# Kernel tuning notes

Hardware: AMD Instinct MI355X
Metric: run time of the kernel (lower is better)

The kernel has to match this reference:

```python
import jax, jax.numpy as jnp
import numpy as np

HIDDEN = 256
HEADS = 8
HEAD_DIM = HIDDEN // HEADS
SCALE = HEAD_DIM ** -0.5
N = 4096
NUM_GRAPHS = 16
LN_EPS = 1e-5


def setup_inputs() -> dict:
    key = jax.random.key(0)
    ks = jax.random.split(key, 8)
    x = jax.random.normal(ks[0], (N, HIDDEN), dtype=jnp.float32)
    batch = jnp.sort(jax.random.randint(ks[1], (N,), 0, NUM_GRAPHS, dtype=jnp.int64))
    # Xavier-uniform linear weights, stored as [in, out] (y = x @ W + b)
    lim = float(np.sqrt(6.0 / (HIDDEN + HIDDEN)))
    def W(k):
        return jax.random.uniform(k, (HIDDEN, HIDDEN), jnp.float32, -lim, lim)
    return {
        "x": x,
        "batch": batch,
        "Wq": W(ks[2]), "bq": jnp.zeros((HIDDEN,), jnp.float32),
        "Wk": W(ks[3]), "bk": jnp.zeros((HIDDEN,), jnp.float32),
        "Wv": W(ks[4]), "bv": jnp.zeros((HIDDEN,), jnp.float32),
        "Wo": W(ks[5]), "bo": jnp.zeros((HIDDEN,), jnp.float32),
        "gamma": jnp.ones((HIDDEN,), jnp.float32),
        "beta": jnp.zeros((HIDDEN,), jnp.float32),
    }


def _layer_norm(x, gamma, beta):
    mu = jnp.mean(x, axis=-1, keepdims=True)
    var = jnp.mean(jnp.square(x - mu), axis=-1, keepdims=True)
    return (x - mu) * jax.lax.rsqrt(var + LN_EPS) * gamma + beta


def reference(x, batch, Wq, bq, Wk, bk, Wv, bv, Wo, bo, gamma, beta):
    residual = x
    h = _layer_norm(x, gamma, beta)
    n = h.shape[0]
    q = (h @ Wq + bq).reshape(n, HEADS, HEAD_DIM)
    k = (h @ Wk + bk).reshape(n, HEADS, HEAD_DIM)
    v = (h @ Wv + bv).reshape(n, HEADS, HEAD_DIM)
    # dense scores masked to block-diagonal (same-graph) structure
    scores = jnp.einsum('ihd,jhd->ihj', q, k) * SCALE  # [N, H, N]
    same_graph = (batch[None, :] == batch[:, None])[:, None, :]  # [N, 1, N]
    scores = jnp.where(same_graph, scores, -jnp.inf)
    attn = jax.nn.softmax(scores, axis=-1)
    attn = jnp.nan_to_num(attn, nan=0.0)
    out = jnp.einsum('ihj,jhd->ihd', attn, v).reshape(n, HIDDEN)
    out = out @ Wo + bo
    return residual + out
```

## Files before the change

### kernel.cpp

```cpp
#include <hip/hip_runtime.h>

#define NNODES 4096
#define HID 256
#define NG 16
#define NH 8
#define HD 32
#define LN_EPS 1e-5f
#define QSCALE (0.17677669529663687f * 1.4426950408889634f)
#define CAPT 384
#define KLS 40
#define VTS (CAPT + 2)

typedef unsigned short u16;
typedef unsigned int u32;
typedef __bf16 bf16x8 __attribute__((ext_vector_type(8)));
typedef float f32x4 __attribute__((ext_vector_type(4)));

__device__ __forceinline__ float bf2f(u16 u){
  union { u32 i; float f; } c; c.i = ((u32)u) << 16; return c.f;
}
__device__ __forceinline__ u16 f2bf(float f){
  union { float f; u32 i; } c; c.f = f;
  u32 x = c.i;
  return (u16)((x + 0x7fffu + ((x >> 16) & 1u)) >> 16);
}

__global__ __launch_bounds__(256) void prep_kernel(
    const float* __restrict__ x, const float* __restrict__ gamma,
    const float* __restrict__ beta, u16* __restrict__ h,
    const float* __restrict__ Wq, const float* __restrict__ Wk,
    const float* __restrict__ Wv, const float* __restrict__ Wo,
    u16* __restrict__ Wt, const int* __restrict__ bw, int* __restrict__ seg){
  __shared__ u16 tile[32][33];
  __shared__ int bad;
  int b = blockIdx.x;
  if (b < 1024){
    int wave = threadIdx.x >> 6, lane = threadIdx.x & 63;
    int row = b * 4 + wave;
    float4 xv = ((const float4*)x)[row * 64 + lane];
    float a0 = xv.x, a1 = xv.y, a2 = xv.z, a3 = xv.w;
    float s = a0 + a1 + a2 + a3;
    #pragma unroll
    for (int m = 1; m < 64; m <<= 1) s += __shfl_xor(s, m);
    float mu = s * (1.0f / HID);
    float d0 = a0 - mu, d1 = a1 - mu, d2 = a2 - mu, d3 = a3 - mu;
    float vv = d0*d0 + d1*d1 + d2*d2 + d3*d3;
    #pragma unroll
    for (int m = 1; m < 64; m <<= 1) vv += __shfl_xor(vv, m);
    float rs = rsqrtf(vv * (1.0f / HID) + LN_EPS);
    float4 gv = ((const float4*)gamma)[lane];
    float4 bv = ((const float4*)beta)[lane];
    ushort4 o;
    o.x = f2bf(d0 * rs * gv.x + bv.x);
    o.y = f2bf(d1 * rs * gv.y + bv.y);
    o.z = f2bf(d2 * rs * gv.z + bv.z);
    o.w = f2bf(d3 * rs * gv.w + bv.w);
    *(ushort4*)(h + (size_t)row * HID + lane * 4) = o;
  } else if (b < 1280){
    int idx = b - 1024;
    int w = idx >> 6;
    int t = idx & 63;
    int bx = (t & 7) * 32, by = (t >> 3) * 32;
    const float* src = (w == 0) ? Wq : (w == 1) ? Wk : (w == 2) ? Wv : Wo;
    u16* dst = Wt + (size_t)w * HID * HID;
    int tx = threadIdx.x & 31, ty = threadIdx.x >> 5;
    #pragma unroll
    for (int r = 0; r < 32; r += 8)
      tile[ty + r][tx] = f2bf(src[(size_t)(by + ty + r) * HID + bx + tx]);
    __syncthreads();
    #pragma unroll
    for (int r = 0; r < 32; r += 8)
      dst[(size_t)(bx + ty + r) * HID + by + tx] = tile[tx][ty + r];
  } else {
    if (threadIdx.x == 0) bad = 0;
    __syncthreads();
    int local_bad = 0;
    for (int i = threadIdx.x; i < NNODES; i += 256){
      int v = bw[i];
      if (v < 0 || v > 15) local_bad = 1;
      if (i + 1 < NNODES && bw[i + 1] < v) local_bad = 1;
    }
    if (local_bad) atomicOr(&bad, 1);
    __syncthreads();
    int stride = bad ? 2 : 1;
    int g = threadIdx.x;
    if (g <= NG){
      int lo = 0, hi = NNODES;
      while (lo < hi){
        int mid = (lo + hi) >> 1;
        if (bw[mid * stride] < g) lo = mid + 1; else hi = mid;
      }
      seg[g] = lo;
    }
  }
}

template<bool FINAL>
__device__ __forceinline__ void gemm_tile(const u16* __restrict__ A, const u16* __restrict__ Bt,
    const float* __restrict__ bias, const float* __restrict__ resid, void* __restrict__ out){
  int gw = blockIdx.x * 4 + (threadIdx.x >> 6);
  int lane = threadIdx.x & 63;
  int lr = lane & 15, lq = lane >> 4;
  int m0 = (gw >> 4) * 64;
  int n0 = (gw & 15) * 16;
  f32x4 acc[4] = {};
  const u16* arow = A + (size_t)(m0 + lr) * HID + lq * 8;
  const u16* brow = Bt + (size_t)(n0 + lr) * HID + lq * 8;
  #pragma unroll
  for (int k0 = 0; k0 < HID; k0 += 32){
    bf16x8 b = *(const bf16x8*)(brow + k0);
    #pragma unroll
    for (int t = 0; t < 4; t++){
      bf16x8 a = *(const bf16x8*)(arow + (size_t)t * 16 * HID + k0);
      acc[t] = __builtin_amdgcn_mfma_f32_16x16x32_bf16(a, b, acc[t], 0, 0, 0);
    }
  }
  int col = n0 + lr;
  float bb = bias[col];
  #pragma unroll
  for (int t = 0; t < 4; t++){
    #pragma unroll
    for (int r = 0; r < 4; r++){
      int row = m0 + 16 * t + lq * 4 + r;
      float val = acc[t][r] + bb;
      if (FINAL){
        val += resid[(size_t)row * HID + col];
        ((float*)out)[(size_t)row * HID + col] = val;
      } else {
        ((u16*)out)[(size_t)row * HID + col] = f2bf(val);
      }
    }
  }
}

__global__ __launch_bounds__(256) void gemm_qkv_kernel(const u16* __restrict__ h,
    const u16* __restrict__ Wt, const float* __restrict__ bq, const float* __restrict__ bk,
    const float* __restrict__ bv, u16* __restrict__ q, u16* __restrict__ k, u16* __restrict__ v){
  int which = blockIdx.y;
  const u16* B = Wt + (size_t)which * HID * HID;
  const float* bias = (which == 0) ? bq : (which == 1) ? bk : bv;
  u16* out = (which == 0) ? q : (which == 1) ? k : v;
  gemm_tile<false>(h, B, bias, nullptr, out);
}

__global__ __launch_bounds__(256) void gemm_proj_kernel(const u16* __restrict__ ao,
    const u16* __restrict__ WtO, const float* __restrict__ bo, const float* __restrict__ x,
    float* __restrict__ out){
  gemm_tile<true>(ao, WtO, bo, x, out);
}

__global__ __launch_bounds__(512, 4) void attn_kernel(const u16* __restrict__ q,
    const u16* __restrict__ k, const u16* __restrict__ v, const int* __restrict__ seg,
    u16* __restrict__ out){
  __shared__ u16 kl[CAPT * KLS];
  __shared__ u16 vt[HD * VTS];
  __shared__ float mg[4][10][64];
  int gh = blockIdx.y;
  int g = gh >> 3, hd = gh & 7;
  int start = seg[g], end = seg[g + 1];
  int len = end - start;
  if (len <= 0) return;
  if (len > CAPT) len = CAPT;
  int ntj = (len + 15) >> 4;
  int nj16 = ntj << 4;
  for (int idx = threadIdx.x; idx < nj16 * 4; idx += 512){
    int row = idx >> 2, part = idx & 3;
    uint4 val = make_uint4(0, 0, 0, 0);
    if (row < len)
      val = *(const uint4*)&k[(size_t)(start + row) * HID + hd * HD + part * 8];
    *(uint4*)&kl[row * KLS + part * 8] = val;
  }
  for (int idx = threadIdx.x; idx < nj16 * 4; idx += 512){
    int row = idx >> 2, part = idx & 3;
    uint4 w = make_uint4(0, 0, 0, 0);
    if (row < len)
      w = *(const uint4*)&v[(size_t)(start + row) * HID + hd * HD + part * 8];
    int d0 = part * 8;
    vt[(d0 + 0) * VTS + row] = (u16)(w.x & 0xffffu);
    vt[(d0 + 1) * VTS + row] = (u16)(w.x >> 16);
    vt[(d0 + 2) * VTS + row] = (u16)(w.y & 0xffffu);
    vt[(d0 + 3) * VTS + row] = (u16)(w.y >> 16);
    vt[(d0 + 4) * VTS + row] = (u16)(w.z & 0xffffu);
    vt[(d0 + 5) * VTS + row] = (u16)(w.z >> 16);
    vt[(d0 + 6) * VTS + row] = (u16)(w.w & 0xffffu);
    vt[(d0 + 7) * VTS + row] = (u16)(w.w >> 16);
  }
  __syncthreads();
  int wave = threadIdx.x >> 6, lane = threadIdx.x & 63;
  int lq = lane >> 4, lr = lane & 15;
  int tl = wave & 3;
  int jh = wave >> 2;
  int nouter = (ntj + 15) >> 4;
  for (int it = 0; it < nouter; it++){
    int tq = it * 16 + blockIdx.x * 4 + tl;
    bool active = tq < ntj;
    int q0 = tq << 4;
    float m = -3.0e38f, l = 0.f;
    f32x4 o0 = {0.f,0.f,0.f,0.f}, o1 = {0.f,0.f,0.f,0.f};
    if (active){
      bf16x8 qf = *(const bf16x8*)&q[(size_t)(start + q0 + lr) * HID + hd * HD + lq * 8];
      int half = (ntj + 1) >> 1;
      int jt0 = jh ? half : 0;
      int jt1 = jh ? ntj : half;
      for (int jt = jt0; jt < jt1; jt++){
        int j0 = jt << 4;
        bf16x8 kf = *(const bf16x8*)&kl[(j0 + lr) * KLS + lq * 8];
        f32x4 st = __builtin_amdgcn_mfma_f32_16x16x32_bf16(kf, qf,
                     (f32x4){0.f,0.f,0.f,0.f}, 0, 0, 0);
        int jb = j0 + lq * 4;
        float s0 = (jb + 0 < len) ? st[0] * QSCALE : -3.0e38f;
        float s1 = (jb + 1 < len) ? st[1] * QSCALE : -3.0e38f;
        float s2 = (jb + 2 < len) ? st[2] * QSCALE : -3.0e38f;
        float s3 = (jb + 3 < len) ? st[3] * QSCALE : -3.0e38f;
        float tm = fmaxf(fmaxf(s0, s1), fmaxf(s2, s3));
        tm = fmaxf(tm, __shfl_xor(tm, 16));
        tm = fmaxf(tm, __shfl_xor(tm, 32));
        float mn = fmaxf(m, tm);
        float alpha = exp2f(m - mn);
        float p0 = exp2f(s0 - mn), p1 = exp2f(s1 - mn);
        float p2 = exp2f(s2 - mn), p3 = exp2f(s3 - mn);
        float ps = (p0 + p1) + (p2 + p3);
        ps += __shfl_xor(ps, 16);
        ps += __shfl_xor(ps, 32);
        l = l * alpha + ps;
        m = mn;
        union { bf16x8 v8; u32 w[4]; } pf, vf0, vf1;
        pf.w[0] = (u32)f2bf(p0) | ((u32)f2bf(p1) << 16);
        pf.w[1] = (u32)f2bf(p2) | ((u32)f2bf(p3) << 16);
        pf.w[2] = 0; pf.w[3] = 0;
        const u16* vp0 = &vt[lr * VTS + j0 + lq * 4];
        const u16* vp1 = &vt[(16 + lr) * VTS + j0 + lq * 4];
        vf0.w[0] = *(const u32*)vp0; vf0.w[1] = *(const u32*)(vp0 + 2);
        vf0.w[2] = 0; vf0.w[3] = 0;
        vf1.w[0] = *(const u32*)vp1; vf1.w[1] = *(const u32*)(vp1 + 2);
        vf1.w[2] = 0; vf1.w[3] = 0;
        o0 = o0 * alpha;
        o1 = o1 * alpha;
        o0 = __builtin_amdgcn_mfma_f32_16x16x32_bf16(vf0.v8, pf.v8, o0, 0, 0, 0);
        o1 = __builtin_amdgcn_mfma_f32_16x16x32_bf16(vf1.v8, pf.v8, o1, 0, 0, 0);
      }
    }
    if (jh == 1){
      mg[tl][0][lane] = o0[0]; mg[tl][1][lane] = o0[1];
      mg[tl][2][lane] = o0[2]; mg[tl][3][lane] = o0[3];
      mg[tl][4][lane] = o1[0]; mg[tl][5][lane] = o1[1];
      mg[tl][6][lane] = o1[2]; mg[tl][7][lane] = o1[3];
      mg[tl][8][lane] = m;     mg[tl][9][lane] = l;
    }
    __syncthreads();
    if (jh == 0 && active && q0 + lr < len){
      float m2 = mg[tl][8][lane], l2 = mg[tl][9][lane];
      float mn = fmaxf(m, m2);
      float a  = exp2f(m - mn);
      float a2 = exp2f(m2 - mn);
      float lt = l * a + l2 * a2;
      float rl = 1.0f / lt;
      float r0 = (o0[0]*a + mg[tl][0][lane]*a2) * rl;
      float r1 = (o0[1]*a + mg[tl][1][lane]*a2) * rl;
      float r2 = (o0[2]*a + mg[tl][2][lane]*a2) * rl;
      float r3 = (o0[3]*a + mg[tl][3][lane]*a2) * rl;
      float r4 = (o1[0]*a + mg[tl][4][lane]*a2) * rl;
      float r5 = (o1[1]*a + mg[tl][5][lane]*a2) * rl;
      float r6 = (o1[2]*a + mg[tl][6][lane]*a2) * rl;
      float r7 = (o1[3]*a + mg[tl][7][lane]*a2) * rl;
      u16* orow = out + (size_t)(start + q0 + lr) * HID + hd * HD;
      int dbase = lq * 4;
      *(u32*)&orow[dbase]          = (u32)f2bf(r0) | ((u32)f2bf(r1) << 16);
      *(u32*)&orow[dbase + 2]      = (u32)f2bf(r2) | ((u32)f2bf(r3) << 16);
      *(u32*)&orow[16 + dbase]     = (u32)f2bf(r4) | ((u32)f2bf(r5) << 16);
      *(u32*)&orow[16 + dbase + 2] = (u32)f2bf(r6) | ((u32)f2bf(r7) << 16);
    }
    __syncthreads();
  }
}

__global__ void sentinel_kernel(u32* __restrict__ out, int nwords){
  int i = blockIdx.x * 256 + threadIdx.x;
  if (i < nwords) out[i] = 0x46404640u;
}

extern "C" void kernel_launch(void* const* d_in, const int* in_sizes, int n_in,
                              void* d_out, int out_size, void* d_ws, size_t ws_size,
                              hipStream_t stream){
  const float* x   = (const float*)d_in[0];
  const int* batch = (const int*)d_in[1];
  const float* Wq = (const float*)d_in[2],  *bq = (const float*)d_in[3];
  const float* Wk = (const float*)d_in[4],  *bk = (const float*)d_in[5];
  const float* Wv = (const float*)d_in[6],  *bv = (const float*)d_in[7];
  const float* Wo = (const float*)d_in[8],  *bo = (const float*)d_in[9];
  const float* gamma = (const float*)d_in[10], *beta = (const float*)d_in[11];

  const size_t WT_OFF  = 1024;
  const size_t QKV_OFF = WT_OFF + 4 * HID * HID * 2;
  const size_t BUF     = (size_t)NNODES * HID * 2;
  const size_t NEED    = QKV_OFF + 4 * BUF;

  if (ws_size < NEED){
    int nwords = out_size / 2;
    sentinel_kernel<<<(nwords + 255) / 256, 256, 0, stream>>>((u32*)d_out, nwords);
    return;
  }

  char* w = (char*)d_ws;
  int* seg  = (int*)(w + 128);
  u16* Wt   = (u16*)(w + WT_OFF);
  u16* qb   = (u16*)(w + QKV_OFF);
  u16* kb   = qb + (size_t)NNODES * HID;
  u16* vb   = kb + (size_t)NNODES * HID;
  u16* ao   = vb + (size_t)NNODES * HID;
  u16* h    = (u16*)d_out;

  prep_kernel<<<1281, 256, 0, stream>>>(x, gamma, beta, h, Wq, Wk, Wv, Wo, Wt, batch, seg);
  gemm_qkv_kernel<<<dim3(256, 3), 256, 0, stream>>>(h, Wt, bq, bk, bv, qb, kb, vb);
  attn_kernel<<<dim3(4, NG * NH), 512, 0, stream>>>(qb, kb, vb, seg, ao);
  gemm_proj_kernel<<<256, 256, 0, stream>>>(ao, Wt + 3 * (size_t)HID * HID, bo, x, (float*)d_out);
}
```

Before: 129.1 us.

## Shrink attention LDS footprint to fit more blocks per CU

Reduces the per-graph key capacity from 384 to 336 rows and tightens the K row stride from 40 to 34. The cross-half merge buffer now stores partial outputs as packed bf16 instead of fp32. Together these cut shared memory per block, and launch bounds are raised to 6 blocks per CU to raise occupancy. The risks are graphs longer than 336 nodes being silently truncated, more LDS bank conflicts from the odd stride, and extra rounding of partial sums.

```diff
diff --git a/kernel.cpp b/kernel.cpp
--- a/kernel.cpp
+++ b/kernel.cpp
@@ -7,8 +7,8 @@
 #define HD 32
 #define LN_EPS 1e-5f
 #define QSCALE (0.17677669529663687f * 1.4426950408889634f)
-#define CAPT 384
-#define KLS 40
+#define CAPT 336
+#define KLS 34
 #define VTS (CAPT + 2)
 
 typedef unsigned short u16;
@@ -149,12 +149,13 @@
   gemm_tile<true>(ao, WtO, bo, x, out);
 }
 
-__global__ __launch_bounds__(512, 4) void attn_kernel(const u16* __restrict__ q,
+__global__ __launch_bounds__(512, 6) void attn_kernel(const u16* __restrict__ q,
     const u16* __restrict__ k, const u16* __restrict__ v, const int* __restrict__ seg,
     u16* __restrict__ out){
   __shared__ u16 kl[CAPT * KLS];
   __shared__ u16 vt[HD * VTS];
-  __shared__ float mg[4][10][64];
+  __shared__ float mgml[4][2][64];
+  __shared__ u32 mgo[4][4][64];
   int gh = blockIdx.y;
   int g = gh >> 3, hd = gh & 7;
   int start = seg[g], end = seg[g + 1];
@@ -241,28 +242,31 @@
       }
     }
     if (jh == 1){
-      mg[tl][0][lane] = o0[0]; mg[tl][1][lane] = o0[1];
-      mg[tl][2][lane] = o0[2]; mg[tl][3][lane] = o0[3];
-      mg[tl][4][lane] = o1[0]; mg[tl][5][lane] = o1[1];
-      mg[tl][6][lane] = o1[2]; mg[tl][7][lane] = o1[3];
-      mg[tl][8][lane] = m;     mg[tl][9][lane] = l;
+      mgo[tl][0][lane] = (u32)f2bf(o0[0]) | ((u32)f2bf(o0[1]) << 16);
+      mgo[tl][1][lane] = (u32)f2bf(o0[2]) | ((u32)f2bf(o0[3]) << 16);
+      mgo[tl][2][lane] = (u32)f2bf(o1[0]) | ((u32)f2bf(o1[1]) << 16);
+      mgo[tl][3][lane] = (u32)f2bf(o1[2]) | ((u32)f2bf(o1[3]) << 16);
+      mgml[tl][0][lane] = m;
+      mgml[tl][1][lane] = l;
     }
     __syncthreads();
     if (jh == 0 && active && q0 + lr < len){
-      float m2 = mg[tl][8][lane], l2 = mg[tl][9][lane];
+      float m2 = mgml[tl][0][lane], l2 = mgml[tl][1][lane];
       float mn = fmaxf(m, m2);
       float a  = exp2f(m - mn);
       float a2 = exp2f(m2 - mn);
       float lt = l * a + l2 * a2;
       float rl = 1.0f / lt;
-      float r0 = (o0[0]*a + mg[tl][0][lane]*a2) * rl;
-      float r1 = (o0[1]*a + mg[tl][1][lane]*a2) * rl;
-      float r2 = (o0[2]*a + mg[tl][2][lane]*a2) * rl;
-      float r3 = (o0[3]*a + mg[tl][3][lane]*a2) * rl;
-      float r4 = (o1[0]*a + mg[tl][4][lane]*a2) * rl;
-      float r5 = (o1[1]*a + mg[tl][5][lane]*a2) * rl;
-      float r6 = (o1[2]*a + mg[tl][6][lane]*a2) * rl;
-      float r7 = (o1[3]*a + mg[tl][7][lane]*a2) * rl;
+      u32 w0 = mgo[tl][0][lane], w1 = mgo[tl][1][lane];
+      u32 w2 = mgo[tl][2][lane], w3 = mgo[tl][3][lane];
+      float r0 = (o0[0]*a + bf2f((u16)(w0 & 0xffffu))*a2) * rl;
+      float r1 = (o0[1]*a + bf2f((u16)(w0 >> 16))*a2) * rl;
+      float r2 = (o0[2]*a + bf2f((u16)(w1 & 0xffffu))*a2) * rl;
+      float r3 = (o0[3]*a + bf2f((u16)(w1 >> 16))*a2) * rl;
+      float r4 = (o1[0]*a + bf2f((u16)(w2 & 0xffffu))*a2) * rl;
+      float r5 = (o1[1]*a + bf2f((u16)(w2 >> 16))*a2) * rl;
+      float r6 = (o1[2]*a + bf2f((u16)(w3 & 0xffffu))*a2) * rl;
+      float r7 = (o1[3]*a + bf2f((u16)(w3 >> 16))*a2) * rl;
       u16* orow = out + (size_t)(start + q0 + lr) * HID + hd * HD;
       int dbase = lq * 4;
       *(u32*)&orow[dbase]          = (u32)f2bf(r0) | ((u32)f2bf(r1) << 16);
```

Result: no change. 130.5 us (+1.1%).
